# Kernel optimization log

Hardware: AMD Instinct MI355X
Metric: run time of the kernel (lower is better)

The kernel has to match this reference:

```python
import jax, jax.numpy as jnp
import numpy as np

EMBED_DIM = 1024
NUM_HEADS = 16
HEAD_DIM = EMBED_DIM // NUM_HEADS


def setup_inputs() -> dict:
    key = jax.random.key(0)
    ks = jax.random.split(key, 7)
    N, L = 2, 2048
    sv = 1.0 / np.sqrt(HEAD_DIM)
    so = 1.0 / np.sqrt(EMBED_DIM)
    return {
        "values": jax.random.normal(ks[0], (N, L, EMBED_DIM), jnp.float32),
        "keys": jax.random.normal(ks[1], (N, L, EMBED_DIM), jnp.float32),
        "query": jax.random.normal(ks[2], (N, L, EMBED_DIM), jnp.float32),
        # NOTE: original torch code applies self.values to v, k AND q; keys/queries
        # Linears are dead parameters, so only Wv/bv and fc_out are materialized.
        "Wv": jax.random.uniform(ks[3], (HEAD_DIM, HEAD_DIM), jnp.float32, -sv, sv),
        "bv": jax.random.uniform(ks[4], (HEAD_DIM,), jnp.float32, -sv, sv),
        "Wo": jax.random.uniform(ks[5], (EMBED_DIM, EMBED_DIM), jnp.float32, -so, so),
        "bo": jax.random.uniform(ks[6], (EMBED_DIM,), jnp.float32, -so, so),
    }


def reference(values, keys, query, Wv, bv, Wo, bo):
    N, Lq, _ = query.shape
    Lk = keys.shape[1]
    Lv = values.shape[1]
    # split heads: (N, L, H, D)
    v = values.reshape(N, Lv, NUM_HEADS, HEAD_DIM)
    k = keys.reshape(N, Lk, NUM_HEADS, HEAD_DIM)
    q = query.reshape(N, Lq, NUM_HEADS, HEAD_DIM)
    # faithful to source: the SAME value projection is applied to v, k, q
    proj = lambda x: jnp.einsum('nlhd,ed->nlhe', x, Wv) + bv
    v = proj(v)
    k = proj(k)
    q = proj(q)
    # energy: (N, H, Q, K); note scaling by sqrt(embed_dim), as in source
    energy = jnp.einsum('nqhd,nkhd->nhqk', q, k)
    attention = jax.nn.softmax(energy / jnp.sqrt(jnp.float32(EMBED_DIM)), axis=3)
    out = jnp.einsum('nhql,nlhd->nqhd', attention, v).reshape(N, Lq, EMBED_DIM)
    return out @ Wo.T + bo
```

## Files before the change

kernel.cpp:

```cpp
#include <hip/hip_runtime.h>

typedef unsigned short u16;
typedef __bf16 bf16x4 __attribute__((ext_vector_type(4)));
typedef __bf16 bf16x8 __attribute__((ext_vector_type(8)));
typedef float  f32x4  __attribute__((ext_vector_type(4)));
typedef float  f32x16 __attribute__((ext_vector_type(16)));

#define MFMA16(a, b, c) __builtin_amdgcn_mfma_f32_16x16x32_bf16((a), (b), (c), 0, 0, 0)
#define MFMA32(a, b, c) __builtin_amdgcn_mfma_f32_32x32x16_bf16((a), (b), (c), 0, 0, 0)


__global__ __launch_bounds__(256) void prep_kernel(
    const float* __restrict__ values, const float* __restrict__ keys,
    const float* __restrict__ query,  const float* __restrict__ Wv,
    const float* __restrict__ bv,     const float* __restrict__ Wo,
    u16* __restrict__ Qb, u16* __restrict__ Kb, u16* __restrict__ VTb,
    u16* __restrict__ Wob) {
    const int b = blockIdx.x;
    const int t = b >> 10;
    if (t == 3) {
        const int i = ((b - 3072) * 256 + threadIdx.x) * 4;
        float4 v = *(const float4*)&Wo[i];
        bf16x4 o = { (__bf16)v.x, (__bf16)v.y, (__bf16)v.z, (__bf16)v.w };
        *(bf16x4*)&Wob[i] = o;
        return;
    }
    __shared__ __align__(16) u16 Wvs[64 * 72];
    __shared__ __align__(16) u16 Xs[64 * 72];
    const int lt = b & 31, h = (b >> 5) & 15, n = (b >> 9) & 1;
    const int nh = n * 16 + h, l0 = lt * 64;
    const int tid = threadIdx.x, wave = tid >> 6, lane = tid & 63;
    const int quad = lane >> 4, l16 = lane & 15;
    const float* xin = (t == 0) ? values : (t == 1 ? keys : query);

#pragma unroll
    for (int j = 0; j < 4; ++j) {
        const int chunk = tid + 256 * j, r = chunk >> 4, c = (chunk & 15) * 4;
        float4 w = *(const float4*)&Wv[r * 64 + c];
        bf16x4 wb = { (__bf16)w.x, (__bf16)w.y, (__bf16)w.z, (__bf16)w.w };
        *(bf16x4*)&Wvs[r * 72 + c] = wb;
        float4 x = *(const float4*)&xin[(size_t)(n * 2048 + l0 + r) * 1024 + h * 64 + c];
        bf16x4 xb = { (__bf16)x.x, (__bf16)x.y, (__bf16)x.z, (__bf16)x.w };
        *(bf16x4*)&Xs[r * 72 + c] = xb;
    }
    __syncthreads();

    bf16x8 wf[4][2], xf[2];
#pragma unroll
    for (int f = 0; f < 4; ++f)
#pragma unroll
        for (int ks = 0; ks < 2; ++ks)
            wf[f][ks] = *(const bf16x8*)&Wvs[(f * 16 + l16) * 72 + ks * 32 + quad * 8];
#pragma unroll
    for (int ks = 0; ks < 2; ++ks)
        xf[ks] = *(const bf16x8*)&Xs[(wave * 16 + l16) * 72 + ks * 32 + quad * 8];

    f32x4 acc[4];
#pragma unroll
    for (int i = 0; i < 4; ++i) acc[i] = (f32x4){0.f, 0.f, 0.f, 0.f};

    if (t == 0) {
#pragma unroll
        for (int nf = 0; nf < 4; ++nf) {
            acc[nf] = MFMA16(xf[0], wf[nf][0], acc[nf]);
            acc[nf] = MFMA16(xf[1], wf[nf][1], acc[nf]);
        }
    } else {
#pragma unroll
        for (int mf = 0; mf < 4; ++mf) {
            acc[mf] = MFMA16(wf[mf][0], xf[0], acc[mf]);
            acc[mf] = MFMA16(wf[mf][1], xf[1], acc[mf]);
        }
    }
    __syncthreads();

    const float scale = (t == 2) ? 0.04508422f : 1.0f;
    if (t == 0) {
#pragma unroll
        for (int nf = 0; nf < 4; ++nf) {
            const float bias = bv[nf * 16 + l16];
            bf16x4 o = { (__bf16)(acc[nf][0] + bias), (__bf16)(acc[nf][1] + bias),
                         (__bf16)(acc[nf][2] + bias), (__bf16)(acc[nf][3] + bias) };
            *(bf16x4*)&Xs[(nf * 16 + l16) * 72 + wave * 16 + quad * 4] = o;
        }
    } else {
#pragma unroll
        for (int mf = 0; mf < 4; ++mf) {
            bf16x4 o = { (__bf16)((acc[mf][0] + bv[mf * 16 + quad * 4 + 0]) * scale),
                         (__bf16)((acc[mf][1] + bv[mf * 16 + quad * 4 + 1]) * scale),
                         (__bf16)((acc[mf][2] + bv[mf * 16 + quad * 4 + 2]) * scale),
                         (__bf16)((acc[mf][3] + bv[mf * 16 + quad * 4 + 3]) * scale) };
            *(bf16x4*)&Xs[(wave * 16 + l16) * 72 + mf * 16 + quad * 4] = o;
        }
    }
    __syncthreads();

    u16* dst = (t == 0) ? VTb : (t == 1 ? Kb : Qb);
#pragma unroll
    for (int j = 0; j < 2; ++j) {
        const int chunk = tid + 256 * j, r = chunk >> 3, c = (chunk & 7) * 8;
        const size_t off = (t == 0) ? (size_t)(nh * 64 + r) * 2048 + l0 + c
                                    : (size_t)(nh * 2048 + l0 + r) * 64 + c;
        *(int4*)&dst[off] = *(const int4*)&Xs[r * 72 + c];
    }
}

__global__ __launch_bounds__(256, 4) void flash_kernel(
    const u16* __restrict__ Qb, const u16* __restrict__ Kb,
    const u16* __restrict__ VTb, float* __restrict__ Opart,
    float* __restrict__ Lp) {
    __shared__ __align__(16) u16 Ks[64 * 72];
    __shared__ __align__(16) u16 Vs[64 * 72];
    __shared__ __align__(16) u16 Ps[4][32 * 72];
    const int b = blockIdx.x;
    const int nh = b >> 5, qsl = (b >> 1) & 15, ks = b & 1;
    const int tid = threadIdx.x, wave = tid >> 6, lane = tid & 63;
    const int l32 = lane & 31, half = lane >> 5;
    const int q0 = qsl * 128 + wave * 32;
    const int s4 = (b >> 1) * 4 + wave;
    u16* Pw = &Ps[wave][0];

    const u16* Qg = Qb + ((size_t)nh * 2048 + q0) * 64;
    bf16x8 qf[4];
#pragma unroll
    for (int kg = 0; kg < 4; ++kg)
        qf[kg] = *(const bf16x8*)&Qg[l32 * 64 + kg * 16 + half * 8];

    f32x16 Oacc[2];
#pragma unroll
    for (int dt = 0; dt < 2; ++dt)
#pragma unroll
        for (int r = 0; r < 16; ++r) Oacc[dt][r] = 0.f;
    float lsum = 0.f;

    const u16* Kg = Kb + (size_t)nh * 2048 * 64;
    const u16* Vg = VTb + (size_t)nh * 64 * 2048;

    for (int kt = 0; kt < 16; ++kt) {
        __syncthreads();
        const int k0 = ks * 1024 + kt * 64;
#pragma unroll
        for (int j = 0; j < 2; ++j) {
            const int chunk = tid + 256 * j, r = chunk >> 3, c = (chunk & 7) * 8;
            *(int4*)&Ks[r * 72 + c] = *(const int4*)&Kg[(size_t)(k0 + r) * 64 + c];
            *(int4*)&Vs[r * 72 + c] = *(const int4*)&Vg[(size_t)r * 2048 + k0 + c];
        }
        __syncthreads();

#pragma unroll
        for (int t2 = 0; t2 < 2; ++t2) {
            f32x16 s;
#pragma unroll
            for (int r = 0; r < 16; ++r) s[r] = 0.f;
#pragma unroll
            for (int kg = 0; kg < 4; ++kg) {
                bf16x8 ak = *(const bf16x8*)&Ks[(t2 * 32 + l32) * 72 + kg * 16 + half * 8];
                s = MFMA32(ak, qf[kg], s);
            }
#pragma unroll
            for (int a = 0; a < 4; ++a) {
                const float p0 = __builtin_amdgcn_exp2f(s[4 * a + 0]);
                const float p1 = __builtin_amdgcn_exp2f(s[4 * a + 1]);
                const float p2 = __builtin_amdgcn_exp2f(s[4 * a + 2]);
                const float p3 = __builtin_amdgcn_exp2f(s[4 * a + 3]);
                lsum += (p0 + p1) + (p2 + p3);
                bf16x4 pk = { (__bf16)p0, (__bf16)p1, (__bf16)p2, (__bf16)p3 };
                *(bf16x4*)&Pw[l32 * 72 + t2 * 32 + a * 8 + half * 4] = pk;
            }
        }

#pragma unroll
        for (int kk = 0; kk < 4; ++kk) {
            bf16x8 bp = *(const bf16x8*)&Pw[l32 * 72 + kk * 16 + half * 8];
#pragma unroll
            for (int dt = 0; dt < 2; ++dt) {
                bf16x8 av = *(const bf16x8*)&Vs[(dt * 32 + l32) * 72 + kk * 16 + half * 8];
                Oacc[dt] = MFMA32(av, bp, Oacc[dt]);
            }
        }
    }

    float* Ob = Opart + ((size_t)s4 * 2 + ks) * 2048;
#pragma unroll
    for (int dt = 0; dt < 2; ++dt)
#pragma unroll
        for (int r = 0; r < 16; ++r)
            Ob[(dt * 16 + r) * 64 + lane] = Oacc[dt][r];
    Lp[((size_t)s4 * 2 + ks) * 64 + lane] = lsum;
}

__global__ __launch_bounds__(256) void combine_kernel(
    const float* __restrict__ Opart, const float* __restrict__ Lp,
    u16* __restrict__ AOb) {
    __shared__ __align__(16) float Ls[64 * 36];
    const int s4 = blockIdx.x;
    const int nh = s4 >> 6, qsl = (s4 >> 2) & 15, w = s4 & 3;
    const int t = threadIdx.x;
    const size_t b0 = (size_t)s4 * 2 * 2048;

#pragma unroll
    for (int jj = 0; jj < 2; ++jj) {
        const int fi = t + jj * 256;
        float4 a = *(const float4*)&Opart[b0 + (size_t)fi * 4];
        float4 c = *(const float4*)&Opart[b0 + 2048 + (size_t)fi * 4];
        float4 sum = { a.x + c.x, a.y + c.y, a.z + c.z, a.w + c.w };
        const int flat = fi * 4, i = flat >> 6, lb = flat & 63;
        const int q = lb & 31, hf = lb >> 5, dtv = i >> 4, r = i & 15;
        const int d = (r & 3) + 8 * (r >> 2) + 4 * hf + 32 * dtv;
        *(float4*)&Ls[d * 36 + q] = sum;
    }
    __syncthreads();

    const int q = t >> 3, dg = t & 7;
    const float ls = Lp[(size_t)s4 * 2 * 64 + q] + Lp[(size_t)s4 * 2 * 64 + 32 + q]
                   + Lp[((size_t)s4 * 2 + 1) * 64 + q] + Lp[((size_t)s4 * 2 + 1) * 64 + 32 + q];
    const float inv = 1.0f / ls;

    bf16x8 o;
#pragma unroll
    for (int i = 0; i < 8; ++i)
        o[i] = (__bf16)(Ls[(dg * 8 + i) * 36 + q] * inv);
    const int row = (nh >> 4) * 2048 + qsl * 128 + w * 32 + q;
    const int col = (nh & 15) * 64 + dg * 8;
    *(bf16x8*)&AOb[(size_t)row * 1024 + col] = o;
}

__global__ __launch_bounds__(256) void out_gemm_kernel(
    const u16* __restrict__ A, const u16* __restrict__ Bw,
    const float* __restrict__ bo, float* __restrict__ out) {
    __shared__ __align__(16) u16 As[128 * 72];
    __shared__ __align__(16) u16 Bs[64 * 72];
    const int b = blockIdx.x, rt = b >> 4, ct = b & 15;
    const int row0 = rt * 128, col0 = ct * 64;
    const int tid = threadIdx.x, wave = tid >> 6, lane = tid & 63;
    const int l32 = lane & 31, half = lane >> 5;

    f32x16 acc[2];
#pragma unroll
    for (int cg = 0; cg < 2; ++cg)
#pragma unroll
        for (int r = 0; r < 16; ++r) acc[cg][r] = 0.f;

    for (int kt = 0; kt < 16; ++kt) {
        __syncthreads();
        const int k0 = kt * 64;
#pragma unroll
        for (int j = 0; j < 4; ++j) {
            const int chunk = tid + 256 * j, r = chunk >> 3, c = (chunk & 7) * 8;
            *(int4*)&As[r * 72 + c] = *(const int4*)&A[(size_t)(row0 + r) * 1024 + k0 + c];
        }
#pragma unroll
        for (int j = 0; j < 2; ++j) {
            const int chunk = tid + 256 * j, r = chunk >> 3, c = (chunk & 7) * 8;
            *(int4*)&Bs[r * 72 + c] = *(const int4*)&Bw[(size_t)(col0 + r) * 1024 + k0 + c];
        }
        __syncthreads();
#pragma unroll
        for (int kg = 0; kg < 4; ++kg) {
            bf16x8 af = *(const bf16x8*)&As[(wave * 32 + l32) * 72 + kg * 16 + half * 8];
#pragma unroll
            for (int cg = 0; cg < 2; ++cg) {
                bf16x8 bf = *(const bf16x8*)&Bs[(cg * 32 + l32) * 72 + kg * 16 + half * 8];
                acc[cg] = MFMA32(af, bf, acc[cg]);
            }
        }
    }

#pragma unroll
    for (int cg = 0; cg < 2; ++cg) {
        const int col = col0 + cg * 32 + l32;
        const float bias = bo[col];
#pragma unroll
        for (int r = 0; r < 16; ++r) {
            const int row = row0 + wave * 32 + (r & 3) + 8 * (r >> 2) + 4 * half;
            out[(size_t)row * 1024 + col] = acc[cg][r] + bias;
        }
    }
}

extern "C" void kernel_launch(void* const* d_in, const int* in_sizes, int n_in,
                              void* d_out, int out_size, void* d_ws, size_t ws_size,
                              hipStream_t stream) {
    (void)in_sizes; (void)n_in; (void)out_size; (void)ws_size;
    const float* values = (const float*)d_in[0];
    const float* keys   = (const float*)d_in[1];
    const float* query  = (const float*)d_in[2];
    const float* Wv     = (const float*)d_in[3];
    const float* bv     = (const float*)d_in[4];
    const float* Wo     = (const float*)d_in[5];
    const float* bo     = (const float*)d_in[6];

    char* ws = (char*)d_ws;
    u16*   Qb    = (u16*)(ws);
    u16*   Kb    = (u16*)(ws + (8ull  << 20));
    u16*   VTb   = (u16*)(ws + (16ull << 20));
    u16*   AOb   = (u16*)(ws + (24ull << 20));
    u16*   Wob   = (u16*)(ws + (32ull << 20));
    float* Opart = (float*)(ws + (34ull << 20));
    float* Lp    = (float*)(ws + (66ull << 20));

    prep_kernel<<<4096, 256, 0, stream>>>(values, keys, query, Wv, bv, Wo,
                                          Qb, Kb, VTb, Wob);
    flash_kernel<<<1024, 256, 0, stream>>>(Qb, Kb, VTb, Opart, Lp);
    combine_kernel<<<2048, 256, 0, stream>>>(Opart, Lp, AOb);
    out_gemm_kernel<<<512, 256, 0, stream>>>(AOb, Wob, bo, (float*)d_out);
}
```

Baseline: 177.5 us.

## Store flash partials as bf16 in output layout, simplify combine, widen out GEMM

The flash kernel now converts its partial output accumulators to bf16, transposes them through the per-wave LDS tile, and writes them directly in the final row-major (token, embed) layout. It also pre-reduces the row sums across the two half-waves. The combine kernel becomes a simple elementwise add-and-scale with no shared-memory transpose, and reads half as many bytes. The output GEMM moves to 512 threads with one 32x32 accumulator per wave, raising wave count per block. The risk is extra rounding, since the unnormalized partials are rounded to bf16 before summation.

```diff
diff --git a/kernel.cpp b/kernel.cpp
--- a/kernel.cpp
+++ b/kernel.cpp
@@ -107,7 +107,7 @@
 
 __global__ __launch_bounds__(256, 4) void flash_kernel(
     const u16* __restrict__ Qb, const u16* __restrict__ Kb,
-    const u16* __restrict__ VTb, float* __restrict__ Opart,
+    const u16* __restrict__ VTb, u16* __restrict__ Op,
     float* __restrict__ Lp) {
     __shared__ __align__(16) u16 Ks[64 * 72];
     __shared__ __align__(16) u16 Vs[64 * 72];
@@ -180,52 +180,48 @@
         }
     }
 
-    float* Ob = Opart + ((size_t)s4 * 2 + ks) * 2048;
+    const float lq = lsum + __shfl_xor(lsum, 32);
+    if (half == 0)
+        Lp[((size_t)s4 * 2 + ks) * 32 + l32] = lq;
+
 #pragma unroll
     for (int dt = 0; dt < 2; ++dt)
 #pragma unroll
-        for (int r = 0; r < 16; ++r)
-            Ob[(dt * 16 + r) * 64 + lane] = Oacc[dt][r];
-    Lp[((size_t)s4 * 2 + ks) * 64 + lane] = lsum;
+        for (int a = 0; a < 4; ++a) {
+            bf16x4 o = { (__bf16)Oacc[dt][4 * a + 0], (__bf16)Oacc[dt][4 * a + 1],
+                         (__bf16)Oacc[dt][4 * a + 2], (__bf16)Oacc[dt][4 * a + 3] };
+            *(bf16x4*)&Pw[l32 * 72 + dt * 32 + a * 8 + half * 4] = o;
+        }
+    u16* Ob = Op + (size_t)ks * 4194304 +
+              ((size_t)(nh >> 4) * 2048 + q0) * 1024 + (nh & 15) * 64;
+#pragma unroll
+    for (int j = 0; j < 4; ++j) {
+        const int chunk = lane + 64 * j, r = chunk >> 3, c = (chunk & 7) * 8;
+        *(int4*)&Ob[(size_t)r * 1024 + c] = *(const int4*)&Pw[r * 72 + c];
+    }
 }
 
 __global__ __launch_bounds__(256) void combine_kernel(
-    const float* __restrict__ Opart, const float* __restrict__ Lp,
+    const u16* __restrict__ Op, const float* __restrict__ Lp,
     u16* __restrict__ AOb) {
-    __shared__ __align__(16) float Ls[64 * 36];
-    const int s4 = blockIdx.x;
-    const int nh = s4 >> 6, qsl = (s4 >> 2) & 15, w = s4 & 3;
-    const int t = threadIdx.x;
-    const size_t b0 = (size_t)s4 * 2 * 2048;
-
-#pragma unroll
-    for (int jj = 0; jj < 2; ++jj) {
-        const int fi = t + jj * 256;
-        float4 a = *(const float4*)&Opart[b0 + (size_t)fi * 4];
-        float4 c = *(const float4*)&Opart[b0 + 2048 + (size_t)fi * 4];
-        float4 sum = { a.x + c.x, a.y + c.y, a.z + c.z, a.w + c.w };
-        const int flat = fi * 4, i = flat >> 6, lb = flat & 63;
-        const int q = lb & 31, hf = lb >> 5, dtv = i >> 4, r = i & 15;
-        const int d = (r & 3) + 8 * (r >> 2) + 4 * hf + 32 * dtv;
-        *(float4*)&Ls[d * 36 + q] = sum;
-    }
-    __syncthreads();
-
-    const int q = t >> 3, dg = t & 7;
-    const float ls = Lp[(size_t)s4 * 2 * 64 + q] + Lp[(size_t)s4 * 2 * 64 + 32 + q]
-                   + Lp[((size_t)s4 * 2 + 1) * 64 + q] + Lp[((size_t)s4 * 2 + 1) * 64 + 32 + q];
-    const float inv = 1.0f / ls;
-
+    const int u = blockIdx.x * 256 + threadIdx.x;
+    const int row = u >> 7, ecol = (u & 127) * 8;
+    const int h = ecol >> 6;
+    const int n = row >> 11, qsl = (row >> 7) & 15, w = (row >> 5) & 3, q = row & 31;
+    const int s4 = (((n * 16 + h) * 16 + qsl) << 2) + w;
+    const float l = Lp[(size_t)s4 * 2 * 32 + q] + Lp[((size_t)s4 * 2 + 1) * 32 + q];
+    const float inv = 1.0f / l;
+    const size_t off = (size_t)row * 1024 + ecol;
+    bf16x8 a = *(const bf16x8*)&Op[off];
+    bf16x8 c = *(const bf16x8*)&Op[4194304 + off];
     bf16x8 o;
 #pragma unroll
     for (int i = 0; i < 8; ++i)
-        o[i] = (__bf16)(Ls[(dg * 8 + i) * 36 + q] * inv);
-    const int row = (nh >> 4) * 2048 + qsl * 128 + w * 32 + q;
-    const int col = (nh & 15) * 64 + dg * 8;
-    *(bf16x8*)&AOb[(size_t)row * 1024 + col] = o;
-}
-
-__global__ __launch_bounds__(256) void out_gemm_kernel(
+        o[i] = (__bf16)(((float)a[i] + (float)c[i]) * inv);
+    *(bf16x8*)&AOb[off] = o;
+}
+
+__global__ __launch_bounds__(512) void out_gemm_kernel(
     const u16* __restrict__ A, const u16* __restrict__ Bw,
     const float* __restrict__ bo, float* __restrict__ out) {
     __shared__ __align__(16) u16 As[128 * 72];
@@ -234,47 +230,39 @@
     const int row0 = rt * 128, col0 = ct * 64;
     const int tid = threadIdx.x, wave = tid >> 6, lane = tid & 63;
     const int l32 = lane & 31, half = lane >> 5;
-
-    f32x16 acc[2];
-#pragma unroll
-    for (int cg = 0; cg < 2; ++cg)
-#pragma unroll
-        for (int r = 0; r < 16; ++r) acc[cg][r] = 0.f;
+    const int wr = wave & 3, wc = wave >> 2;
+
+    f32x16 acc;
+#pragma unroll
+    for (int r = 0; r < 16; ++r) acc[r] = 0.f;
 
     for (int kt = 0; kt < 16; ++kt) {
         __syncthreads();
         const int k0 = kt * 64;
 #pragma unroll
-        for (int j = 0; j < 4; ++j) {
-            const int chunk = tid + 256 * j, r = chunk >> 3, c = (chunk & 7) * 8;
+        for (int j = 0; j < 2; ++j) {
+            const int chunk = tid + 512 * j, r = chunk >> 3, c = (chunk & 7) * 8;
             *(int4*)&As[r * 72 + c] = *(const int4*)&A[(size_t)(row0 + r) * 1024 + k0 + c];
         }
-#pragma unroll
-        for (int j = 0; j < 2; ++j) {
-            const int chunk = tid + 256 * j, r = chunk >> 3, c = (chunk & 7) * 8;
+        {
+            const int r = tid >> 3, c = (tid & 7) * 8;
             *(int4*)&Bs[r * 72 + c] = *(const int4*)&Bw[(size_t)(col0 + r) * 1024 + k0 + c];
         }
         __syncthreads();
 #pragma unroll
         for (int kg = 0; kg < 4; ++kg) {
-            bf16x8 af = *(const bf16x8*)&As[(wave * 32 + l32) * 72 + kg * 16 + half * 8];
-#pragma unroll
-            for (int cg = 0; cg < 2; ++cg) {
-                bf16x8 bf = *(const bf16x8*)&Bs[(cg * 32 + l32) * 72 + kg * 16 + half * 8];
-                acc[cg] = MFMA32(af, bf, acc[cg]);
-            }
-        }
-    }
-
-#pragma unroll
-    for (int cg = 0; cg < 2; ++cg) {
-        const int col = col0 + cg * 32 + l32;
-        const float bias = bo[col];
-#pragma unroll
-        for (int r = 0; r < 16; ++r) {
-            const int row = row0 + wave * 32 + (r & 3) + 8 * (r >> 2) + 4 * half;
-            out[(size_t)row * 1024 + col] = acc[cg][r] + bias;
-        }
+            bf16x8 af = *(const bf16x8*)&As[(wr * 32 + l32) * 72 + kg * 16 + half * 8];
+            bf16x8 bf = *(const bf16x8*)&Bs[(wc * 32 + l32) * 72 + kg * 16 + half * 8];
+            acc = MFMA32(af, bf, acc);
+        }
+    }
+
+    const int col = col0 + wc * 32 + l32;
+    const float bias = bo[col];
+#pragma unroll
+    for (int r = 0; r < 16; ++r) {
+        const int row = row0 + wr * 32 + (r & 3) + 8 * (r >> 2) + 4 * half;
+        out[(size_t)row * 1024 + col] = acc[r] + bias;
     }
 }
 
@@ -291,17 +279,17 @@
     const float* bo     = (const float*)d_in[6];
 
     char* ws = (char*)d_ws;
-    u16*   Qb    = (u16*)(ws);
-    u16*   Kb    = (u16*)(ws + (8ull  << 20));
-    u16*   VTb   = (u16*)(ws + (16ull << 20));
-    u16*   AOb   = (u16*)(ws + (24ull << 20));
-    u16*   Wob   = (u16*)(ws + (32ull << 20));
-    float* Opart = (float*)(ws + (34ull << 20));
-    float* Lp    = (float*)(ws + (66ull << 20));
+    u16*   Qb  = (u16*)(ws);
+    u16*   Kb  = (u16*)(ws + (8ull  << 20));
+    u16*   VTb = (u16*)(ws + (16ull << 20));
+    u16*   AOb = (u16*)(ws + (24ull << 20));
+    u16*   Wob = (u16*)(ws + (32ull << 20));
+    u16*   Op  = (u16*)(ws + (34ull << 20));
+    float* Lp  = (float*)(ws + (50ull << 20));
 
     prep_kernel<<<4096, 256, 0, stream>>>(values, keys, query, Wv, bv, Wo,
                                           Qb, Kb, VTb, Wob);
-    flash_kernel<<<1024, 256, 0, stream>>>(Qb, Kb, VTb, Opart, Lp);
-    combine_kernel<<<2048, 256, 0, stream>>>(Opart, Lp, AOb);
-    out_gemm_kernel<<<512, 256, 0, stream>>>(AOb, Wob, bo, (float*)d_out);
-}
+    flash_kernel<<<1024, 256, 0, stream>>>(Qb, Kb, VTb, Op, Lp);
+    combine_kernel<<<2048, 256, 0, stream>>>(Op, Lp, AOb);
+    out_gemm_kernel<<<512, 512, 0, stream>>>(AOb, Wob, bo, (float*)d_out);
+}
```

Measured after the change: 166.9 us. -5.9%, faster.
